# Optimization experiments

Hardware: AMD Instinct MI355X
Metric: run time of the kernel (lower is better)

## Reference

```python
import jax, jax.numpy as jnp
import numpy as np

D_MODEL = 512
N_HEADS = 8
D_K = D_MODEL // N_HEADS
D_FF = 2048
EPS = 1e-5  # torch LayerNorm default


def _layer_norm(x, g, b):
    mu = jnp.mean(x, axis=-1, keepdims=True)
    var = jnp.mean(jnp.square(x - mu), axis=-1, keepdims=True)
    return (x - mu) * jax.lax.rsqrt(var + EPS) * g + b


def setup_inputs() -> dict:
    key = jax.random.key(0)
    ks = jax.random.split(key, 16)
    s_in = 1.0 / np.sqrt(D_MODEL)
    s_ff = 1.0 / np.sqrt(D_FF)
    # Linear weights stored as [in, out] (transpose of torch convention)
    return {
        "x": jax.random.normal(ks[0], (2, 2048, D_MODEL), jnp.float32),
        "wq_w": jax.random.uniform(ks[1], (D_MODEL, D_MODEL), jnp.float32, -s_in, s_in),
        "wq_b": jax.random.uniform(ks[2], (D_MODEL,), jnp.float32, -s_in, s_in),
        "wk_w": jax.random.uniform(ks[3], (D_MODEL, D_MODEL), jnp.float32, -s_in, s_in),
        "wk_b": jax.random.uniform(ks[4], (D_MODEL,), jnp.float32, -s_in, s_in),
        "wv_w": jax.random.uniform(ks[5], (D_MODEL, D_MODEL), jnp.float32, -s_in, s_in),
        "wv_b": jax.random.uniform(ks[6], (D_MODEL,), jnp.float32, -s_in, s_in),
        "wo_w": jax.random.uniform(ks[7], (D_MODEL, D_MODEL), jnp.float32, -s_in, s_in),
        "wo_b": jax.random.uniform(ks[8], (D_MODEL,), jnp.float32, -s_in, s_in),
        "ln1_g": jnp.ones((D_MODEL,), jnp.float32),
        "ln1_b": jnp.zeros((D_MODEL,), jnp.float32),
        "fc1_w": jax.random.uniform(ks[9], (D_MODEL, D_FF), jnp.float32, -s_in, s_in),
        "fc1_b": jax.random.uniform(ks[10], (D_FF,), jnp.float32, -s_in, s_in),
        "fc2_w": jax.random.uniform(ks[11], (D_FF, D_MODEL), jnp.float32, -s_ff, s_ff),
        "fc2_b": jax.random.uniform(ks[12], (D_MODEL,), jnp.float32, -s_ff, s_ff),
        "ln2_g": jnp.ones((D_MODEL,), jnp.float32),
        "ln2_b": jnp.zeros((D_MODEL,), jnp.float32),
    }


def reference(x, wq_w, wq_b, wk_w, wk_b, wv_w, wv_b, wo_w, wo_b,
              ln1_g, ln1_b, fc1_w, fc1_b, fc2_w, fc2_b, ln2_g, ln2_b):
    B, T, _ = x.shape
    # --- multi-head self-attention (mask=None; dropout in eval mode = identity) ---
    q = (x @ wq_w + wq_b).reshape(B, T, N_HEADS, D_K).transpose(0, 2, 1, 3)  # [B,H,T,d_k]
    k = (x @ wk_w + wk_b).reshape(B, T, N_HEADS, D_K).transpose(0, 2, 1, 3)
    v = (x @ wv_w + wv_b).reshape(B, T, N_HEADS, D_K).transpose(0, 2, 1, 3)
    scores = jnp.einsum("bhqd,bhkd->bhqk", q, k) / np.sqrt(D_K).astype(np.float32)
    attn = jax.nn.softmax(scores, axis=-1)  # [B,H,T,T]
    ctx = jnp.einsum("bhqk,bhkd->bhqd", attn, v)
    ctx = ctx.transpose(0, 2, 1, 3).reshape(B, T, D_MODEL)
    attn_out = ctx @ wo_w + wo_b
    # --- residual + LN1 ---
    h = _layer_norm(x + attn_out, ln1_g, ln1_b)
    # --- FFN (relu) + residual + LN2 ---
    ffn = jax.nn.relu(h @ fc1_w + fc1_b) @ fc2_w + fc2_b
    out = _layer_norm(h + ffn, ln2_g, ln2_b)
    return out, attn
```

## Files before the change

kernel.cpp:

```cpp
#include <hip/hip_runtime.h>
#include <hip/hip_bf16.h>

typedef __hip_bfloat16 bf16;
typedef __attribute__((ext_vector_type(8))) short short8v;
typedef __attribute__((ext_vector_type(4))) float f32x4;

#define B_   2
#define T_   2048
#define D_   512
#define H_   8
#define DK_  64
#define DFF_ 2048
#define M_   (B_*T_)

static __device__ __forceinline__ float b2f(bf16 v) { return __bfloat162float(v); }
static __device__ __forceinline__ bf16  f2b(float v){ return __float2bfloat16(v); }

static __device__ __forceinline__ float ldin(const void* p, size_t i, bool bf) {
    return bf ? __bfloat162float(((const bf16*)p)[i]) : ((const float*)p)[i];
}
static __device__ __forceinline__ void stout(void* p, size_t i, float v, bool bf) {
    if (bf) ((bf16*)p)[i] = __float2bfloat16(v);
    else    ((float*)p)[i] = v;
}

__global__ void detect_dtype(const unsigned int* __restrict__ x, int* __restrict__ flag)
{
    __shared__ int cnt;
    if (threadIdx.x == 0) cnt = 0;
    __syncthreads();
    int local = 0;
    for (int i = threadIdx.x; i < 1024; i += 256) {
        unsigned int lo = x[i] & 0xFFFFu;
        float v = __uint_as_float(lo << 16);
        float a = fabsf(v);
        if (a > 1e-3f && a < 16.f) local++;
    }
    atomicAdd(&cnt, local);
    __syncthreads();
    if (threadIdx.x == 0) *flag = (cnt > 512) ? 1 : 0;
}

__global__ __launch_bounds__(256)
void transpose_w(const void* __restrict__ W, bf16* __restrict__ oh,
                 bf16* __restrict__ ol, const int* __restrict__ flag,
                 int K, int N, float scale)
{
    const bool bf = (*flag != 0);
    __shared__ float tile[32][33];
    const int n0 = blockIdx.x * 32;
    const int k0 = blockIdx.y * 32;
    const int c  = threadIdx.x & 31;
    const int r8 = threadIdx.x >> 5;

    #pragma unroll
    for (int i = 0; i < 4; ++i) {
        int r = r8 + i * 8;
        tile[r][c] = ldin(W, (size_t)(k0 + r) * N + n0 + c, bf) * scale;
    }
    __syncthreads();
    #pragma unroll
    for (int i = 0; i < 4; ++i) {
        int r = r8 + i * 8;
        float v = tile[c][r];
        bf16 h = f2b(v);
        oh[(size_t)(n0 + r) * K + k0 + c] = h;
        if (!bf) ol[(size_t)(n0 + r) * K + k0 + c] = f2b(v - b2f(h));
    }
}

__global__ __launch_bounds__(256)
void transpose_b(const bf16* __restrict__ Vb, bf16* __restrict__ VT)
{
    __shared__ float tile[32][33];
    const int m0 = blockIdx.x * 32;
    const int d0 = blockIdx.y * 32;
    const int c  = threadIdx.x & 31;
    const int r8 = threadIdx.x >> 5;
    #pragma unroll
    for (int i = 0; i < 4; ++i) {
        int r = r8 + i * 8;
        tile[r][c] = b2f(Vb[(size_t)(m0 + r) * D_ + d0 + c]);
    }
    __syncthreads();
    #pragma unroll
    for (int i = 0; i < 4; ++i) {
        int r = r8 + i * 8;
        VT[(size_t)(d0 + r) * M_ + m0 + c] = f2b(tile[c][r]);
    }
}

template<int AFLAG, int RELU, int OBF>
__global__ __launch_bounds__(256)
void gemm_mfma(const void* __restrict__ A,
               const bf16* __restrict__ BTh, const bf16* __restrict__ BTl,
               const void* __restrict__ bias, const int* __restrict__ flag,
               void* __restrict__ C, int M, int N, int K, float bscale)
{
    const bool bfw = (*flag != 0);
    const bool bfa = AFLAG ? bfw : false;

    __shared__ short Ah[64][40];
    __shared__ short Al[64][40];
    __shared__ short Bh[64][40];
    __shared__ short Bl[64][40];

    const int tid  = threadIdx.x;
    const int lane = tid & 63;
    const int wave = tid >> 6;
    const int wm   = wave >> 1;
    const int wn   = wave & 1;
    const int rowBase = blockIdx.y * 64;
    const int colBase = blockIdx.x * 64;

    const int srow = tid >> 2;
    const int skc  = (tid & 3) * 8;

    f32x4 acc[2][2] = {};

    for (int k0 = 0; k0 < K; k0 += 32) {
        __syncthreads();
        if (bfa) {
            const short8v av = *(const short8v*)((const bf16*)A +
                                 (size_t)(rowBase + srow) * K + k0 + skc);
            *(short8v*)&Ah[srow][skc] = av;
        } else {
            const float* Af = (const float*)A + (size_t)(rowBase + srow) * K + k0 + skc;
            const float4 f0 = *(const float4*)(Af);
            const float4 f1 = *(const float4*)(Af + 4);
            const float vals[8] = {f0.x, f0.y, f0.z, f0.w, f1.x, f1.y, f1.z, f1.w};
            short8v hi, lo;
            #pragma unroll
            for (int j = 0; j < 8; ++j) {
                bf16 h = f2b(vals[j]);
                hi[j] = *(const short*)&h;
                bf16 l = f2b(vals[j] - b2f(h));
                lo[j] = *(const short*)&l;
            }
            *(short8v*)&Ah[srow][skc] = hi;
            *(short8v*)&Al[srow][skc] = lo;
        }
        {
            const short8v bh = *(const short8v*)(BTh +
                                 (size_t)(colBase + srow) * K + k0 + skc);
            *(short8v*)&Bh[srow][skc] = bh;
            if (!bfw) {
                const short8v bl = *(const short8v*)(BTl +
                                     (size_t)(colBase + srow) * K + k0 + skc);
                *(short8v*)&Bl[srow][skc] = bl;
            }
        }
        __syncthreads();

        const int fr = lane & 15;
        const int kb = (lane >> 4) * 8;
        short8v aH[2], aL[2], bH[2], bL[2];
        #pragma unroll
        for (int f = 0; f < 2; ++f) {
            aH[f] = *(const short8v*)&Ah[wm * 32 + f * 16 + fr][kb];
            bH[f] = *(const short8v*)&Bh[wn * 32 + f * 16 + fr][kb];
        }
        if (!bfa) {
            #pragma unroll
            for (int f = 0; f < 2; ++f)
                aL[f] = *(const short8v*)&Al[wm * 32 + f * 16 + fr][kb];
        }
        if (!bfw) {
            #pragma unroll
            for (int f = 0; f < 2; ++f)
                bL[f] = *(const short8v*)&Bl[wn * 32 + f * 16 + fr][kb];
        }

        #pragma unroll
        for (int i = 0; i < 2; ++i)
            #pragma unroll
            for (int j = 0; j < 2; ++j) {
                acc[i][j] = __builtin_amdgcn_mfma_f32_16x16x32_bf16(aH[i], bH[j], acc[i][j], 0, 0, 0);
                if (!bfa)
                    acc[i][j] = __builtin_amdgcn_mfma_f32_16x16x32_bf16(aL[i], bH[j], acc[i][j], 0, 0, 0);
                if (!bfw)
                    acc[i][j] = __builtin_amdgcn_mfma_f32_16x16x32_bf16(aH[i], bL[j], acc[i][j], 0, 0, 0);
            }
    }

    const int fr = lane & 15;
    const int rq = (lane >> 4) * 4;
    #pragma unroll
    for (int j = 0; j < 2; ++j) {
        const int col = colBase + wn * 32 + j * 16 + fr;
        const float bv = ldin(bias, col, bfw) * bscale;
        #pragma unroll
        for (int i = 0; i < 2; ++i) {
            #pragma unroll
            for (int q = 0; q < 4; ++q) {
                float v = acc[i][j][q] + bv;
                if (RELU) v = fmaxf(v, 0.f);
                size_t idx = (size_t)(rowBase + wm * 32 + i * 16 + rq + q) * N + col;
                if (OBF) ((bf16*)C)[idx] = f2b(v);
                else     ((float*)C)[idx] = v;
            }
        }
    }
}

__global__ __launch_bounds__(256)
void attn_mfma(const bf16* __restrict__ Qb, const bf16* __restrict__ Kb,
               const bf16* __restrict__ VTb, void* __restrict__ dout,
               const int* __restrict__ flag, float* __restrict__ ctx)
{
    const bool bf = (*flag != 0);
    const int tid  = threadIdx.x;
    const int lane = tid & 63;
    const int wave = tid >> 6;
    const int wm = wave >> 1, wn = wave & 1;
    const int q0 = blockIdx.x * 64;
    const int h  = blockIdx.y;
    const int b  = blockIdx.z;
    const size_t OFFOUT = (size_t)M_ * D_;

    __shared__ short Qs[64][72];
    __shared__ short Ks[64][72];
    __shared__ short Vs[64][72];
    __shared__ short Ps[64][72];
    __shared__ float Lp[2][64];
    __shared__ float invl_s[64];

    const int fr = lane & 15;
    const int kb = (lane >> 4) * 8;

    #pragma unroll
    for (int l = 0; l < 2; ++l) {
        int idx = tid + l * 256;
        int r = idx >> 3, c8 = (idx & 7) * 8;
        *(short8v*)&Qs[r][c8] =
            *(const short8v*)(Qb + (size_t)(b*T_ + q0 + r) * D_ + h*DK_ + c8);
    }

    float lsum[2][4] = {};

    for (int kt = 0; kt < T_/64; ++kt) {
        __syncthreads();
        #pragma unroll
        for (int l = 0; l < 2; ++l) {
            int idx = tid + l * 256;
            int r = idx >> 3, c8 = (idx & 7) * 8;
            *(short8v*)&Ks[r][c8] =
                *(const short8v*)(Kb + (size_t)(b*T_ + kt*64 + r) * D_ + h*DK_ + c8);
        }
        __syncthreads();

        short8v aF[2][2], bF[2][2];
        #pragma unroll
        for (int i = 0; i < 2; ++i)
            #pragma unroll
            for (int k2 = 0; k2 < 2; ++k2)
                aF[i][k2] = *(const short8v*)&Qs[wm*32 + i*16 + fr][kb + k2*32];
        #pragma unroll
        for (int j = 0; j < 2; ++j)
            #pragma unroll
            for (int k2 = 0; k2 < 2; ++k2)
                bF[j][k2] = *(const short8v*)&Ks[wn*32 + j*16 + fr][kb + k2*32];

        #pragma unroll
        for (int i = 0; i < 2; ++i)
            #pragma unroll
            for (int j = 0; j < 2; ++j) {
                f32x4 s = {};
                s = __builtin_amdgcn_mfma_f32_16x16x32_bf16(aF[i][0], bF[j][0], s, 0, 0, 0);
                s = __builtin_amdgcn_mfma_f32_16x16x32_bf16(aF[i][1], bF[j][1], s, 0, 0, 0);
                #pragma unroll
                for (int q = 0; q < 4; ++q)
                    lsum[i][q] += __expf(fminf(s[q], 60.f));
            }
    }

    #pragma unroll
    for (int i = 0; i < 2; ++i)
        #pragma unroll
        for (int q = 0; q < 4; ++q) {
            float v = lsum[i][q];
            #pragma unroll
            for (int o = 8; o; o >>= 1) v += __shfl_xor(v, o, 16);
            lsum[i][q] = v;
        }
    if (fr == 0) {
        #pragma unroll
        for (int i = 0; i < 2; ++i)
            #pragma unroll
            for (int q = 0; q < 4; ++q)
                Lp[wn][wm*32 + i*16 + (lane>>4)*4 + q] = lsum[i][q];
    }
    __syncthreads();
    if (tid < 64) invl_s[tid] = 1.f / (Lp[0][tid] + Lp[1][tid]);
    __syncthreads();

    float il[2][4];
    #pragma unroll
    for (int i = 0; i < 2; ++i)
        #pragma unroll
        for (int q = 0; q < 4; ++q)
            il[i][q] = invl_s[wm*32 + i*16 + (lane>>4)*4 + q];

    f32x4 cacc[2][2] = {};

    for (int kt = 0; kt < T_/64; ++kt) {
        __syncthreads();
        #pragma unroll
        for (int l = 0; l < 2; ++l) {
            int idx = tid + l * 256;
            int r = idx >> 3, c8 = (idx & 7) * 8;
            *(short8v*)&Ks[r][c8] =
                *(const short8v*)(Kb + (size_t)(b*T_ + kt*64 + r) * D_ + h*DK_ + c8);
            *(short8v*)&Vs[r][c8] =
                *(const short8v*)(VTb + (size_t)(h*DK_ + r) * M_ + b*T_ + kt*64 + c8);
        }
        __syncthreads();

        short8v aF[2][2], bF[2][2];
        #pragma unroll
        for (int i = 0; i < 2; ++i)
            #pragma unroll
            for (int k2 = 0; k2 < 2; ++k2)
                aF[i][k2] = *(const short8v*)&Qs[wm*32 + i*16 + fr][kb + k2*32];
        #pragma unroll
        for (int j = 0; j < 2; ++j)
            #pragma unroll
            for (int k2 = 0; k2 < 2; ++k2)
                bF[j][k2] = *(const short8v*)&Ks[wn*32 + j*16 + fr][kb + k2*32];

        f32x4 sacc[2][2];
        #pragma unroll
        for (int i = 0; i < 2; ++i)
            #pragma unroll
            for (int j = 0; j < 2; ++j) {
                f32x4 s = {};
                s = __builtin_amdgcn_mfma_f32_16x16x32_bf16(aF[i][0], bF[j][0], s, 0, 0, 0);
                s = __builtin_amdgcn_mfma_f32_16x16x32_bf16(aF[i][1], bF[j][1], s, 0, 0, 0);
                sacc[i][j] = s;
            }

        #pragma unroll
        for (int i = 0; i < 2; ++i)
            #pragma unroll
            for (int j = 0; j < 2; ++j) {
                #pragma unroll
                for (int q = 0; q < 4; ++q) {
                    const int qq = wm*32 + i*16 + (lane>>4)*4 + q;
                    const int kk = wn*32 + j*16 + fr;
                    float p = __expf(fminf(sacc[i][j][q], 60.f)) * il[i][q];
                    bf16 pb = f2b(p);
                    Ps[qq][kk] = *(const short*)&pb;
                    size_t go = OFFOUT + ((size_t)((b*H_+h)*T_ + q0 + qq))*T_ + kt*64 + kk;
                    if (bf) ((bf16*)dout)[go] = pb;
                    else    ((float*)dout)[go] = p;
                }
            }
        __syncthreads();

        short8v pF[2][2], vF[2][2];
        #pragma unroll
        for (int i = 0; i < 2; ++i)
            #pragma unroll
            for (int k2 = 0; k2 < 2; ++k2)
                pF[i][k2] = *(const short8v*)&Ps[wm*32 + i*16 + fr][kb + k2*32];
        #pragma unroll
        for (int j = 0; j < 2; ++j)
            #pragma unroll
            for (int k2 = 0; k2 < 2; ++k2)
                vF[j][k2] = *(const short8v*)&Vs[wn*32 + j*16 + fr][kb + k2*32];

        #pragma unroll
        for (int i = 0; i < 2; ++i)
            #pragma unroll
            for (int j = 0; j < 2; ++j) {
                cacc[i][j] = __builtin_amdgcn_mfma_f32_16x16x32_bf16(pF[i][0], vF[j][0], cacc[i][j], 0, 0, 0);
                cacc[i][j] = __builtin_amdgcn_mfma_f32_16x16x32_bf16(pF[i][1], vF[j][1], cacc[i][j], 0, 0, 0);
            }
    }

    #pragma unroll
    for (int i = 0; i < 2; ++i)
        #pragma unroll
        for (int j = 0; j < 2; ++j)
            #pragma unroll
            for (int q = 0; q < 4; ++q) {
                const int qq = wm*32 + i*16 + (lane>>4)*4 + q;
                ctx[(size_t)(b*T_ + q0 + qq)*D_ + h*DK_ + wn*32 + j*16 + fr] = cacc[i][j][q];
            }
}

__global__ __launch_bounds__(256)
void ln1_kernel(const void* X, const float* __restrict__ A,
                const void* g, const void* be,
                const int* __restrict__ flag, float* __restrict__ out)
{
    const bool bf = (*flag != 0);
    const int row = blockIdx.x;
    const int tid = threadIdx.x;
    const size_t base = (size_t)row * D_;

    float v0 = ldin(X, base + tid, bf)       + A[base + tid];
    float v1 = ldin(X, base + 256 + tid, bf) + A[base + 256 + tid];
    float s  = v0 + v1;
    float sq = v0*v0 + v1*v1;
    #pragma unroll
    for (int o = 32; o; o >>= 1) { s += __shfl_xor(s, o, 64); sq += __shfl_xor(sq, o, 64); }

    __shared__ float rs[4], rq[4];
    if ((tid & 63) == 0) { rs[tid >> 6] = s; rq[tid >> 6] = sq; }
    __syncthreads();
    s  = rs[0] + rs[1] + rs[2] + rs[3];
    sq = rq[0] + rq[1] + rq[2] + rq[3];

    float mu   = s * (1.f / D_);
    float var  = sq * (1.f / D_) - mu * mu;
    float rstd = rsqrtf(var + 1e-5f);
    out[base + tid]       = (v0 - mu) * rstd * ldin(g, tid, bf)       + ldin(be, tid, bf);
    out[base + 256 + tid] = (v1 - mu) * rstd * ldin(g, 256 + tid, bf) + ldin(be, 256 + tid, bf);
}

__global__ __launch_bounds__(256)
void ln2_kernel(const float* __restrict__ Hf, const float* __restrict__ F,
                const void* g, const void* be,
                const int* __restrict__ flag, void* out)
{
    const bool bf = (*flag != 0);
    const int row = blockIdx.x;
    const int tid = threadIdx.x;
    const size_t base = (size_t)row * D_;

    float v0 = Hf[base + tid]       + F[base + tid];
    float v1 = Hf[base + 256 + tid] + F[base + 256 + tid];
    float s  = v0 + v1;
    float sq = v0*v0 + v1*v1;
    #pragma unroll
    for (int o = 32; o; o >>= 1) { s += __shfl_xor(s, o, 64); sq += __shfl_xor(sq, o, 64); }

    __shared__ float rs[4], rq[4];
    if ((tid & 63) == 0) { rs[tid >> 6] = s; rq[tid >> 6] = sq; }
    __syncthreads();
    s  = rs[0] + rs[1] + rs[2] + rs[3];
    sq = rq[0] + rq[1] + rq[2] + rq[3];

    float mu   = s * (1.f / D_);
    float var  = sq * (1.f / D_) - mu * mu;
    float rstd = rsqrtf(var + 1e-5f);
    stout(out, base + tid,       (v0 - mu) * rstd * ldin(g, tid, bf)       + ldin(be, tid, bf),       bf);
    stout(out, base + 256 + tid, (v1 - mu) * rstd * ldin(g, 256 + tid, bf) + ldin(be, 256 + tid, bf), bf);
}

extern "C" void kernel_launch(void* const* d_in, const int* in_sizes, int n_in,
                              void* d_out, int out_size, void* d_ws, size_t ws_size,
                              hipStream_t stream)
{
    const void* x     = d_in[0];
    const void* wq_w  = d_in[1];
    const void* wq_b  = d_in[2];
    const void* wk_w  = d_in[3];
    const void* wk_b  = d_in[4];
    const void* wv_w  = d_in[5];
    const void* wv_b  = d_in[6];
    const void* wo_w  = d_in[7];
    const void* wo_b  = d_in[8];
    const void* ln1_g = d_in[9];
    const void* ln1_b = d_in[10];
    const void* fc1_w = d_in[11];
    const void* fc1_b = d_in[12];
    const void* fc2_w = d_in[13];
    const void* fc2_b = d_in[14];
    const void* ln2_g = d_in[15];
    const void* ln2_b = d_in[16];

    float* ws       = (float*)d_ws;
    const size_t SL = (size_t)M_ * D_;
    bf16*  Qb       = (bf16*)ws;
    bf16*  VTb      = Qb + SL;
    bf16*  Kb       = (bf16*)(ws + SL);
    bf16*  Vb       = (bf16*)(ws + 2*SL);
    float* ctx      = ws + 3*SL;
    float* h        = ws + 4*SL;
    float* ffn2     = ws + 5*SL;
    float* ffn1     = ws;
    int*   flag     = (int*)(ffn2 + SL);

    bf16*  tw   = (bf16*)(flag + 64);
    const size_t SW = (size_t)D_ * D_;
    const size_t SF = (size_t)D_ * DFF_;
    bf16* wqTh = tw;                 bf16* wqTl = wqTh + SW;
    bf16* wkTh = wqTl + SW;          bf16* wkTl = wkTh + SW;
    bf16* wvTh = wkTl + SW;          bf16* wvTl = wvTh + SW;
    bf16* woTh = wvTl + SW;          bf16* woTl = woTh + SW;
    bf16* f1Th = woTl + SW;          bf16* f1Tl = f1Th + SF;
    bf16* f2Th = f1Tl + SF;          bf16* f2Tl = f2Th + SF;

    dim3 blk(256);

    detect_dtype<<<1, 256, 0, stream>>>((const unsigned int*)x, flag);

    transpose_w<<<dim3(D_/32,   D_/32),   blk, 0, stream>>>(wq_w,  wqTh, wqTl, flag, D_,   D_,   0.125f);
    transpose_w<<<dim3(D_/32,   D_/32),   blk, 0, stream>>>(wk_w,  wkTh, wkTl, flag, D_,   D_,   1.f);
    transpose_w<<<dim3(D_/32,   D_/32),   blk, 0, stream>>>(wv_w,  wvTh, wvTl, flag, D_,   D_,   1.f);
    transpose_w<<<dim3(D_/32,   D_/32),   blk, 0, stream>>>(wo_w,  woTh, woTl, flag, D_,   D_,   1.f);
    transpose_w<<<dim3(DFF_/32, D_/32),   blk, 0, stream>>>(fc1_w, f1Th, f1Tl, flag, D_,   DFF_, 1.f);
    transpose_w<<<dim3(D_/32,   DFF_/32), blk, 0, stream>>>(fc2_w, f2Th, f2Tl, flag, DFF_, D_,   1.f);

    gemm_mfma<1,0,1><<<dim3(D_/64,  M_/64), blk, 0, stream>>>(x, wqTh, wqTl, wq_b, flag, Qb, M_, D_, D_, 0.125f);
    gemm_mfma<1,0,1><<<dim3(D_/64,  M_/64), blk, 0, stream>>>(x, wkTh, wkTl, wk_b, flag, Kb, M_, D_, D_, 1.f);
    gemm_mfma<1,0,1><<<dim3(D_/64,  M_/64), blk, 0, stream>>>(x, wvTh, wvTl, wv_b, flag, Vb, M_, D_, D_, 1.f);

    transpose_b<<<dim3(M_/32, D_/32), blk, 0, stream>>>(Vb, VTb);

    attn_mfma<<<dim3(T_/64, H_, B_), blk, 0, stream>>>(Qb, Kb, VTb, d_out, flag, ctx);

    gemm_mfma<0,0,0><<<dim3(D_/64,  M_/64), blk, 0, stream>>>(ctx, woTh, woTl, wo_b, flag, h, M_, D_, D_, 1.f);

    ln1_kernel<<<M_, 256, 0, stream>>>(x, h, ln1_g, ln1_b, flag, h);

    gemm_mfma<0,1,0><<<dim3(DFF_/64, M_/64), blk, 0, stream>>>(h,    f1Th, f1Tl, fc1_b, flag, ffn1, M_, DFF_, D_, 1.f);
    gemm_mfma<0,0,0><<<dim3(D_/64,   M_/64), blk, 0, stream>>>(ffn1, f2Th, f2Tl, fc2_b, flag, ffn2, M_, D_, DFF_, 1.f);

    ln2_kernel<<<M_, 256, 0, stream>>>(h, ffn2, ln2_g, ln2_b, flag, d_out);
}
```

Baseline: 653.9 us.

## Pre-split activations into bf16 hi/lo, enlarge GEMM tiles, fuse V transpose

```diff
diff --git a/kernel.cpp b/kernel.cpp
--- a/kernel.cpp
+++ b/kernel.cpp
@@ -23,6 +23,15 @@
     if (bf) ((bf16*)p)[i] = __float2bfloat16(v);
     else    ((float*)p)[i] = v;
 }
+static __device__ __forceinline__ short hi_of(float v) {
+    bf16 h = f2b(v);
+    return *(const short*)&h;
+}
+static __device__ __forceinline__ short lo_of(float v) {
+    bf16 h = f2b(v);
+    bf16 l = f2b(v - b2f(h));
+    return *(const short*)&l;
+}
 
 __global__ void detect_dtype(const unsigned int* __restrict__ x, int* __restrict__ flag)
 {
@@ -42,6 +51,32 @@
 }
 
 __global__ __launch_bounds__(256)
+void split_x(const void* __restrict__ X, bf16* __restrict__ xh,
+             bf16* __restrict__ xl, const int* __restrict__ flag)
+{
+    const bool bf = (*flag != 0);
+    const size_t i = ((size_t)blockIdx.x * 256 + threadIdx.x) * 8;
+    if (bf) {
+        *(short8v*)(xh + i) = *(const short8v*)((const bf16*)X + i);
+    } else {
+        const float* Xf = (const float*)X + i;
+        const float4 f0 = *(const float4*)(Xf);
+        const float4 f1 = *(const float4*)(Xf + 4);
+        const float vals[8] = {f0.x, f0.y, f0.z, f0.w, f1.x, f1.y, f1.z, f1.w};
+        short8v hi, lo;
+        #pragma unroll
+        for (int j = 0; j < 8; ++j) {
+            short th = hi_of(vals[j]);
+            short tl = lo_of(vals[j]);
+            hi[j] = th;
+            lo[j] = tl;
+        }
+        *(short8v*)(xh + i) = hi;
+        *(short8v*)(xl + i) = lo;
+    }
+}
+
+__global__ __launch_bounds__(256)
 void transpose_w(const void* __restrict__ W, bf16* __restrict__ oh,
                  bf16* __restrict__ ol, const int* __restrict__ flag,
                  int K, int N, float scale)
@@ -69,135 +104,123 @@
     }
 }
 
+template<int BN, int NA, int RELU, int OBF>
 __global__ __launch_bounds__(256)
-void transpose_b(const bf16* __restrict__ Vb, bf16* __restrict__ VT)
-{
-    __shared__ float tile[32][33];
-    const int m0 = blockIdx.x * 32;
-    const int d0 = blockIdx.y * 32;
-    const int c  = threadIdx.x & 31;
-    const int r8 = threadIdx.x >> 5;
-    #pragma unroll
-    for (int i = 0; i < 4; ++i) {
-        int r = r8 + i * 8;
-        tile[r][c] = b2f(Vb[(size_t)(m0 + r) * D_ + d0 + c]);
-    }
-    __syncthreads();
-    #pragma unroll
-    for (int i = 0; i < 4; ++i) {
-        int r = r8 + i * 8;
-        VT[(size_t)(d0 + r) * M_ + m0 + c] = f2b(tile[c][r]);
-    }
-}
-
-template<int AFLAG, int RELU, int OBF>
-__global__ __launch_bounds__(256)
-void gemm_mfma(const void* __restrict__ A,
+void gemm_mfma(const bf16* __restrict__ Ahg, const bf16* __restrict__ Alg,
                const bf16* __restrict__ BTh, const bf16* __restrict__ BTl,
                const void* __restrict__ bias, const int* __restrict__ flag,
-               void* __restrict__ C, int M, int N, int K, float bscale)
-{
-    const bool bfw = (*flag != 0);
-    const bool bfa = AFLAG ? bfw : false;
-
-    __shared__ short Ah[64][40];
-    __shared__ short Al[64][40];
-    __shared__ short Bh[64][40];
-    __shared__ short Bl[64][40];
+               void* __restrict__ C, bf16* __restrict__ Cl,
+               int M, int N, int K, float bscale)
+{
+    constexpr int BM = 128;
+    constexpr int FM = 4;
+    constexpr int FN = BN / 32;
+    const bool bfw   = (*flag != 0);
+    const bool useAl = !(NA == 1 && bfw);
+    const bool useBl = !bfw;
+
+    __shared__ short As[2][BM][40];
+    __shared__ short Bs[2][BN][40];
 
     const int tid  = threadIdx.x;
     const int lane = tid & 63;
     const int wave = tid >> 6;
     const int wm   = wave >> 1;
     const int wn   = wave & 1;
-    const int rowBase = blockIdx.y * 64;
-    const int colBase = blockIdx.x * 64;
-
-    const int srow = tid >> 2;
-    const int skc  = (tid & 3) * 8;
-
-    f32x4 acc[2][2] = {};
+    const int rowBase = blockIdx.y * BM;
+    const int colBase = blockIdx.x * BN;
+
+    const int fr = lane & 15;
+    const int kb = (lane >> 4) * 8;
+
+    const int arow = tid >> 1;
+    const int acol = (tid & 1) * 16;
+    const int brow = (BN == 128) ? (tid >> 1) : (tid >> 2);
+    const int bcol = (BN == 128) ? ((tid & 1) * 16) : ((tid & 3) * 8);
+
+    const bf16* aHs = Ahg + (size_t)(rowBase + arow) * K + acol;
+    const bf16* aLs = Alg + (size_t)(rowBase + arow) * K + acol;
+    const bf16* bHs = BTh + (size_t)(colBase + brow) * K + bcol;
+    const bf16* bLs = BTl + (size_t)(colBase + brow) * K + bcol;
+
+    f32x4 acc[FM][FN] = {};
 
     for (int k0 = 0; k0 < K; k0 += 32) {
         __syncthreads();
-        if (bfa) {
-            const short8v av = *(const short8v*)((const bf16*)A +
-                                 (size_t)(rowBase + srow) * K + k0 + skc);
-            *(short8v*)&Ah[srow][skc] = av;
+        *(short8v*)&As[0][arow][acol]     = *(const short8v*)(aHs + k0);
+        *(short8v*)&As[0][arow][acol + 8] = *(const short8v*)(aHs + k0 + 8);
+        if (useAl) {
+            *(short8v*)&As[1][arow][acol]     = *(const short8v*)(aLs + k0);
+            *(short8v*)&As[1][arow][acol + 8] = *(const short8v*)(aLs + k0 + 8);
+        }
+        if (BN == 128) {
+            *(short8v*)&Bs[0][brow][bcol]     = *(const short8v*)(bHs + k0);
+            *(short8v*)&Bs[0][brow][bcol + 8] = *(const short8v*)(bHs + k0 + 8);
+            if (useBl) {
+                *(short8v*)&Bs[1][brow][bcol]     = *(const short8v*)(bLs + k0);
+                *(short8v*)&Bs[1][brow][bcol + 8] = *(const short8v*)(bLs + k0 + 8);
+            }
         } else {
-            const float* Af = (const float*)A + (size_t)(rowBase + srow) * K + k0 + skc;
-            const float4 f0 = *(const float4*)(Af);
-            const float4 f1 = *(const float4*)(Af + 4);
-            const float vals[8] = {f0.x, f0.y, f0.z, f0.w, f1.x, f1.y, f1.z, f1.w};
-            short8v hi, lo;
-            #pragma unroll
-            for (int j = 0; j < 8; ++j) {
-                bf16 h = f2b(vals[j]);
-                hi[j] = *(const short*)&h;
-                bf16 l = f2b(vals[j] - b2f(h));
-                lo[j] = *(const short*)&l;
-            }
-            *(short8v*)&Ah[srow][skc] = hi;
-            *(short8v*)&Al[srow][skc] = lo;
-        }
-        {
-            const short8v bh = *(const short8v*)(BTh +
-                                 (size_t)(colBase + srow) * K + k0 + skc);
-            *(short8v*)&Bh[srow][skc] = bh;
-            if (!bfw) {
-                const short8v bl = *(const short8v*)(BTl +
-                                     (size_t)(colBase + srow) * K + k0 + skc);
-                *(short8v*)&Bl[srow][skc] = bl;
-            }
-        }
-        __syncthreads();
-
-        const int fr = lane & 15;
-        const int kb = (lane >> 4) * 8;
-        short8v aH[2], aL[2], bH[2], bL[2];
-        #pragma unroll
-        for (int f = 0; f < 2; ++f) {
-            aH[f] = *(const short8v*)&Ah[wm * 32 + f * 16 + fr][kb];
-            bH[f] = *(const short8v*)&Bh[wn * 32 + f * 16 + fr][kb];
-        }
-        if (!bfa) {
-            #pragma unroll
-            for (int f = 0; f < 2; ++f)
-                aL[f] = *(const short8v*)&Al[wm * 32 + f * 16 + fr][kb];
-        }
-        if (!bfw) {
-            #pragma unroll
-            for (int f = 0; f < 2; ++f)
-                bL[f] = *(const short8v*)&Bl[wn * 32 + f * 16 + fr][kb];
-        }
-
-        #pragma unroll
-        for (int i = 0; i < 2; ++i)
-            #pragma unroll
-            for (int j = 0; j < 2; ++j) {
+            *(short8v*)&Bs[0][brow][bcol] = *(const short8v*)(bHs + k0);
+            if (useBl)
+                *(short8v*)&Bs[1][brow][bcol] = *(const short8v*)(bLs + k0);
+        }
+        __syncthreads();
+
+        short8v aH[FM], aL[FM], bH[FN], bL[FN];
+        #pragma unroll
+        for (int f = 0; f < FM; ++f)
+            aH[f] = *(const short8v*)&As[0][wm * 64 + f * 16 + fr][kb];
+        if (useAl) {
+            #pragma unroll
+            for (int f = 0; f < FM; ++f)
+                aL[f] = *(const short8v*)&As[1][wm * 64 + f * 16 + fr][kb];
+        }
+        #pragma unroll
+        for (int f = 0; f < FN; ++f)
+            bH[f] = *(const short8v*)&Bs[0][wn * (BN/2) + f * 16 + fr][kb];
+        if (useBl) {
+            #pragma unroll
+            for (int f = 0; f < FN; ++f)
+                bL[f] = *(const short8v*)&Bs[1][wn * (BN/2) + f * 16 + fr][kb];
+        }
+
+        #pragma unroll
+        for (int i = 0; i < FM; ++i)
+            #pragma unroll
+            for (int j = 0; j < FN; ++j) {
                 acc[i][j] = __builtin_amdgcn_mfma_f32_16x16x32_bf16(aH[i], bH[j], acc[i][j], 0, 0, 0);
-                if (!bfa)
+                if (useAl)
                     acc[i][j] = __builtin_amdgcn_mfma_f32_16x16x32_bf16(aL[i], bH[j], acc[i][j], 0, 0, 0);
-                if (!bfw)
+                if (useBl)
                     acc[i][j] = __builtin_amdgcn_mfma_f32_16x16x32_bf16(aH[i], bL[j], acc[i][j], 0, 0, 0);
             }
     }
 
-    const int fr = lane & 15;
     const int rq = (lane >> 4) * 4;
     #pragma unroll
-    for (int j = 0; j < 2; ++j) {
-        const int col = colBase + wn * 32 + j * 16 + fr;
+    for (int j = 0; j < FN; ++j) {
+        const int col = colBase + wn * (BN/2) + j * 16 + fr;
         const float bv = ldin(bias, col, bfw) * bscale;
         #pragma unroll
-        for (int i = 0; i < 2; ++i) {
+        for (int i = 0; i < FM; ++i) {
             #pragma unroll
             for (int q = 0; q < 4; ++q) {
                 float v = acc[i][j][q] + bv;
                 if (RELU) v = fmaxf(v, 0.f);
-                size_t idx = (size_t)(rowBase + wm * 32 + i * 16 + rq + q) * N + col;
-                if (OBF) ((bf16*)C)[idx] = f2b(v);
-                else     ((float*)C)[idx] = v;
+                const int row = rowBase + wm * 64 + i * 16 + rq + q;
+                if (OBF == 0) {
+                    ((float*)C)[(size_t)row * N + col] = v;
+                } else if (OBF == 1) {
+                    ((bf16*)C)[(size_t)row * N + col] = f2b(v);
+                } else if (OBF == 2) {
+                    size_t idx = (size_t)row * N + col;
+                    bf16 h = f2b(v);
+                    ((bf16*)C)[idx] = h;
+                    Cl[idx] = f2b(v - b2f(h));
+                } else {
+                    ((bf16*)C)[(size_t)col * M + row] = f2b(v);
+                }
             }
         }
     }
@@ -206,7 +229,8 @@
 __global__ __launch_bounds__(256)
 void attn_mfma(const bf16* __restrict__ Qb, const bf16* __restrict__ Kb,
                const bf16* __restrict__ VTb, void* __restrict__ dout,
-               const int* __restrict__ flag, float* __restrict__ ctx)
+               const int* __restrict__ flag,
+               bf16* __restrict__ ctxh, bf16* __restrict__ ctxl)
 {
     const bool bf = (*flag != 0);
     const int tid  = threadIdx.x;
@@ -385,14 +409,19 @@
             #pragma unroll
             for (int q = 0; q < 4; ++q) {
                 const int qq = wm*32 + i*16 + (lane>>4)*4 + q;
-                ctx[(size_t)(b*T_ + q0 + qq)*D_ + h*DK_ + wn*32 + j*16 + fr] = cacc[i][j][q];
+                size_t idx = (size_t)(b*T_ + q0 + qq)*D_ + h*DK_ + wn*32 + j*16 + fr;
+                float v = cacc[i][j][q];
+                bf16 hh = f2b(v);
+                ctxh[idx] = hh;
+                ctxl[idx] = f2b(v - b2f(hh));
             }
 }
 
 __global__ __launch_bounds__(256)
 void ln1_kernel(const void* X, const float* __restrict__ A,
                 const void* g, const void* be,
-                const int* __restrict__ flag, float* __restrict__ out)
+                const int* __restrict__ flag, float* __restrict__ out,
+                bf16* __restrict__ hh, bf16* __restrict__ hl)
 {
     const bool bf = (*flag != 0);
     const int row = blockIdx.x;
@@ -415,8 +444,12 @@
     float mu   = s * (1.f / D_);
     float var  = sq * (1.f / D_) - mu * mu;
     float rstd = rsqrtf(var + 1e-5f);
-    out[base + tid]       = (v0 - mu) * rstd * ldin(g, tid, bf)       + ldin(be, tid, bf);
-    out[base + 256 + tid] = (v1 - mu) * rstd * ldin(g, 256 + tid, bf) + ldin(be, 256 + tid, bf);
+    float y0 = (v0 - mu) * rstd * ldin(g, tid, bf)       + ldin(be, tid, bf);
+    float y1 = (v1 - mu) * rstd * ldin(g, 256 + tid, bf) + ldin(be, 256 + tid, bf);
+    out[base + tid]       = y0;
+    out[base + 256 + tid] = y1;
+    bf16 h0 = f2b(y0); hh[base + tid] = h0;       hl[base + tid]       = f2b(y0 - b2f(h0));
+    bf16 h1 = f2b(y1); hh[base + 256 + tid] = h1; hl[base + 256 + tid] = f2b(y1 - b2f(h1));
 }
 
 __global__ __launch_bounds__(256)
@@ -471,19 +504,23 @@
     const void* ln2_g = d_in[15];
     const void* ln2_b = d_in[16];
 
-    float* ws       = (float*)d_ws;
-    const size_t SL = (size_t)M_ * D_;
-    bf16*  Qb       = (bf16*)ws;
-    bf16*  VTb      = Qb + SL;
-    bf16*  Kb       = (bf16*)(ws + SL);
-    bf16*  Vb       = (bf16*)(ws + 2*SL);
-    float* ctx      = ws + 3*SL;
-    float* h        = ws + 4*SL;
-    float* ffn2     = ws + 5*SL;
-    float* ffn1     = ws;
-    int*   flag     = (int*)(ffn2 + SL);
-
-    bf16*  tw   = (bf16*)(flag + 64);
+    char* W = (char*)d_ws;
+    const size_t MB = 1u << 20;
+    bf16*  xh    = (bf16*)(W + 0*MB);
+    bf16*  xl    = (bf16*)(W + 4*MB);
+    bf16*  Qb    = (bf16*)(W + 8*MB);
+    bf16*  Kb    = (bf16*)(W + 12*MB);
+    bf16*  VTb   = (bf16*)(W + 16*MB);
+    bf16*  ctxh  = (bf16*)(W + 20*MB);
+    bf16*  ctxl  = (bf16*)(W + 24*MB);
+    bf16*  ffn1h = (bf16*)(W + 0*MB);
+    bf16*  ffn1l = (bf16*)(W + 16*MB);
+    float* ao    = (float*)(W + 32*MB);
+    float* ffn2  = (float*)(W + 32*MB);
+    float* h     = (float*)(W + 40*MB);
+    bf16*  hh    = (bf16*)(W + 48*MB);
+    bf16*  hl    = (bf16*)(W + 52*MB);
+    bf16*  tw    = (bf16*)(W + 56*MB);
     const size_t SW = (size_t)D_ * D_;
     const size_t SF = (size_t)D_ * DFF_;
     bf16* wqTh = tw;                 bf16* wqTl = wqTh + SW;
@@ -492,6 +529,7 @@
     bf16* woTh = wvTl + SW;          bf16* woTl = woTh + SW;
     bf16* f1Th = woTl + SW;          bf16* f1Tl = f1Th + SF;
     bf16* f2Th = f1Tl + SF;          bf16* f2Tl = f2Th + SF;
+    int*  flag = (int*)(f2Tl + SF);
 
     dim3 blk(256);
 
@@ -504,20 +542,20 @@
     transpose_w<<<dim3(DFF_/32, D_/32),   blk, 0, stream>>>(fc1_w, f1Th, f1Tl, flag, D_,   DFF_, 1.f);
     transpose_w<<<dim3(D_/32,   DFF_/32), blk, 0, stream>>>(fc2_w, f2Th, f2Tl, flag, DFF_, D_,   1.f);
 
-    gemm_mfma<1,0,1><<<dim3(D_/64,  M_/64), blk, 0, stream>>>(x, wqTh, wqTl, wq_b, flag, Qb, M_, D_, D_, 0.125f);
-    gemm_mfma<1,0,1><<<dim3(D_/64,  M_/64), blk, 0, stream>>>(x, wkTh, wkTl, wk_b, flag, Kb, M_, D_, D_, 1.f);
-    gemm_mfma<1,0,1><<<dim3(D_/64,  M_/64), blk, 0, stream>>>(x, wvTh, wvTl, wv_b, flag, Vb, M_, D_, D_, 1.f);
-
-    transpose_b<<<dim3(M_/32, D_/32), blk, 0, stream>>>(Vb, VTb);
-
-    attn_mfma<<<dim3(T_/64, H_, B_), blk, 0, stream>>>(Qb, Kb, VTb, d_out, flag, ctx);
-
-    gemm_mfma<0,0,0><<<dim3(D_/64,  M_/64), blk, 0, stream>>>(ctx, woTh, woTl, wo_b, flag, h, M_, D_, D_, 1.f);
-
-    ln1_kernel<<<M_, 256, 0, stream>>>(x, h, ln1_g, ln1_b, flag, h);
-
-    gemm_mfma<0,1,0><<<dim3(DFF_/64, M_/64), blk, 0, stream>>>(h,    f1Th, f1Tl, fc1_b, flag, ffn1, M_, DFF_, D_, 1.f);
-    gemm_mfma<0,0,0><<<dim3(D_/64,   M_/64), blk, 0, stream>>>(ffn1, f2Th, f2Tl, fc2_b, flag, ffn2, M_, D_, DFF_, 1.f);
+    split_x<<<(M_*D_)/(256*8), blk, 0, stream>>>(x, xh, xl, flag);
+
+    gemm_mfma<64,1,0,1><<<dim3(D_/64,  M_/128), blk, 0, stream>>>(xh, xl, wqTh, wqTl, wq_b, flag, Qb,  nullptr, M_, D_, D_, 0.125f);
+    gemm_mfma<64,1,0,1><<<dim3(D_/64,  M_/128), blk, 0, stream>>>(xh, xl, wkTh, wkTl, wk_b, flag, Kb,  nullptr, M_, D_, D_, 1.f);
+    gemm_mfma<64,1,0,3><<<dim3(D_/64,  M_/128), blk, 0, stream>>>(xh, xl, wvTh, wvTl, wv_b, flag, VTb, nullptr, M_, D_, D_, 1.f);
+
+    attn_mfma<<<dim3(T_/64, H_, B_), blk, 0, stream>>>(Qb, Kb, VTb, d_out, flag, ctxh, ctxl);
+
+    gemm_mfma<64,0,0,0><<<dim3(D_/64,  M_/128), blk, 0, stream>>>(ctxh, ctxl, woTh, woTl, wo_b, flag, ao, nullptr, M_, D_, D_, 1.f);
+
+    ln1_kernel<<<M_, 256, 0, stream>>>(x, ao, ln1_g, ln1_b, flag, h, hh, hl);
+
+    gemm_mfma<128,0,1,2><<<dim3(DFF_/128, M_/128), blk, 0, stream>>>(hh, hl, f1Th, f1Tl, fc1_b, flag, ffn1h, ffn1l, M_, DFF_, D_, 1.f);
+    gemm_mfma<64,0,0,0><<<dim3(D_/64,   M_/128), blk, 0, stream>>>(ffn1h, ffn1l, f2Th, f2Tl, fc2_b, flag, ffn2, nullptr, M_, D_, DFF_, 1.f);
 
     ln2_kernel<<<M_, 256, 0, stream>>>(h, ffn2, ln2_g, ln2_b, flag, d_out);
 }
```

Result: slower. 686.1 us (+4.9%).
